# Kernel tuning notes

Measured on AMD Instinct MI355X. Metric: run time of the kernel, lower is better.

Reference implementation:

```python
import jax, jax.numpy as jnp
import numpy as np

B, S, D = 4, 4096, 1024

def setup_inputs() -> dict:
    key = jax.random.key(0)
    ks = jax.random.split(key, 11)
    scale = 1.0 / np.sqrt(D)
    def lin(k):
        return jax.random.normal(k, (D, D), dtype=jnp.float32) * scale
    return {
        "x": jax.random.normal(ks[0], (B, S, D), dtype=jnp.float32),
        "Wq": lin(ks[1]), "bq": jax.random.normal(ks[2], (D,), dtype=jnp.float32) * 0.02,
        "Wk": lin(ks[3]), "bk": jax.random.normal(ks[4], (D,), dtype=jnp.float32) * 0.02,
        "Wv": lin(ks[5]), "bv": jax.random.normal(ks[6], (D,), dtype=jnp.float32) * 0.02,
        "W1": lin(ks[7]), "b1": jax.random.normal(ks[8], (D,), dtype=jnp.float32) * 0.02,
        "W2": lin(ks[9]), "b2": jax.random.normal(ks[10], (D,), dtype=jnp.float32) * 0.02,
    }

def reference(x, Wq, bq, Wk, bk, Wv, bv, W1, b1, W2, b2):
    d = x.shape[-1]
    # Single-head self-attention with residual (faithful to source)
    q = x @ Wq + bq  # [B,S,D]
    k = x @ Wk + bk
    v = x @ Wv + bv
    scores = jnp.einsum('bsd,btd->bst', q, k) / jnp.sqrt(jnp.float32(d))  # [B,S,S]
    attn = jax.nn.softmax(scores, axis=-1)
    x = x + jnp.einsum('bst,btd->bsd', attn, v)
    # FeedForward: fc2(relu(fc1(x))), then doubled (x = x + x in source)
    h = jax.nn.relu(x @ W1 + b1)
    y = h @ W2 + b2
    return y + y
```

## Files before the change

### kernel.cpp

```cpp
#include <hip/hip_runtime.h>
#include <stdint.h>

typedef unsigned short u16;
typedef __bf16 bf16x8 __attribute__((ext_vector_type(8)));
typedef float f32x4 __attribute__((ext_vector_type(4)));
typedef unsigned short u16x8 __attribute__((ext_vector_type(8)));
typedef unsigned short u16x4 __attribute__((ext_vector_type(4)));

__device__ __forceinline__ float b2f(u16 b) {
    return __uint_as_float(((unsigned)b) << 16);
}
__device__ __forceinline__ u16 f2b(float f) {
    unsigned u = __float_as_uint(f);
    unsigned r = (u + 0x7fffu + ((u >> 16) & 1u)) >> 16;
    return (u16)r;
}

#define GLDS16(g, l) __builtin_amdgcn_global_load_lds(                        \
    (const __attribute__((address_space(1))) void*)(g),                       \
    (__attribute__((address_space(3))) void*)(l), 16, 0, 0)

#define BAR()  __builtin_amdgcn_s_barrier()
#define LG0()  do { asm volatile("s_waitcnt lgkmcnt(0)" ::: "memory");        \
                    __builtin_amdgcn_sched_barrier(0); } while (0)
#define VMC(n) asm volatile("s_waitcnt vmcnt(" #n ")" ::: "memory")

template<int HAS_BIAS, int RELU, int HAS_RES, int OUT_MODE>
__device__ __forceinline__ void gemm8_body(
    const u16* __restrict__ A, const u16* __restrict__ Bt,
    const float* __restrict__ bias, const float* __restrict__ res,
    void* __restrict__ Cout, int N, int K,
    long sA, long sB, long sC, long sR, float scale)
{
    __shared__ u16 smem[65536];

    const long nwg = (long)gridDim.x * gridDim.y * gridDim.z;
    long gid = ((long)blockIdx.z * gridDim.y + blockIdx.y) * gridDim.x + blockIdx.x;
    long logical = (nwg % 8 == 0) ? (gid & 7) * (nwg >> 3) + (gid >> 3) : gid;
    const int bx = (int)(logical % gridDim.x);
    long tmp = logical / gridDim.x;
    const int by = (int)(tmp % gridDim.y);
    const int bz = (int)(tmp / gridDim.y);

    A  += (long)bz * sA;
    Bt += (long)bz * sB;

    const int tid  = threadIdx.x;
    const int lane = tid & 63, wid = tid >> 6;
    const int wm   = wid >> 2, wn = wid & 3;
    const int lr   = lane & 15, lk = lane >> 4;
    const long m0  = (long)by * 256;
    const long n0  = (long)bx * 256;
    const int  NT  = K >> 6;

    const u16* gA0 = A  + (m0 + (tid >> 2)) * (long)K + (tid & 3) * 8;
    const u16* gB0 = Bt + (n0 + (tid >> 2)) * (long)K + (tid & 3) * 8;
    const u16* gA1 = gA0 + 128L * K;
    const u16* gB1 = gB0 + 128L * K;
    const int wdst = (tid & ~63) * 8;

#define STA(bufn, kk, kof) do {                                               \
    GLDS16(gA0 + (kof) + (kk) * 32, &smem[(bufn)*16384 + (kk)*8192 + wdst]);  \
    GLDS16(gA1 + (kof) + (kk) * 32, &smem[(bufn)*16384 + (kk)*8192 + wdst + 4096]); } while (0)
#define STB(bufn, kk, kof) do {                                               \
    GLDS16(gB0 + (kof) + (kk) * 32, &smem[32768 + (bufn)*16384 + (kk)*8192 + wdst]); \
    GLDS16(gB1 + (kof) + (kk) * 32, &smem[32768 + (bufn)*16384 + (kk)*8192 + wdst + 4096]); } while (0)

    const int raOff = (wm * 128 + lr) * 32 + lk * 8;
    const int rbOff = (wn * 64  + lr) * 32 + lk * 8;

#define LDA(kk, ih) do { _Pragma("unroll")                                    \
    for (int i = 0; i < 4; ++i)                                               \
        a[i] = *(const bf16x8*)&smem[cur*16384 + (kk)*8192 + raOff + ((ih)*4 + i)*512]; } while (0)
#define LDB(kk) do { _Pragma("unroll")                                        \
    for (int j = 0; j < 4; ++j)                                               \
        b[j] = *(const bf16x8*)&smem[32768 + cur*16384 + (kk)*8192 + rbOff + j*512]; } while (0)
#define MF(ih) do { __builtin_amdgcn_s_setprio(1); _Pragma("unroll")          \
    for (int i = 0; i < 4; ++i) _Pragma("unroll")                             \
        for (int j = 0; j < 4; ++j)                                           \
            acc[(ih)*4 + i][j] = __builtin_amdgcn_mfma_f32_16x16x32_bf16(     \
                a[i], b[j], acc[(ih)*4 + i][j], 0, 0, 0);                     \
    __builtin_amdgcn_s_setprio(0); } while (0)

    f32x4 acc[8][4];
    #pragma unroll
    for (int i = 0; i < 8; ++i)
        #pragma unroll
        for (int j = 0; j < 4; ++j)
            #pragma unroll
            for (int r = 0; r < 4; ++r) acc[i][j][r] = 0.0f;

    bf16x8 a[4], b[4];

    STA(0, 0, 0); STB(0, 0, 0); STA(0, 1, 0); STB(0, 1, 0);
    VMC(4);
    BAR();

    int cur = 0;
    #pragma unroll 1
    for (int t = 0; t < NT - 1; ++t) {
        const long kof = (long)(t + 1) * 64;
        const int nxt = cur ^ 1;
        LDA(0, 0); LDB(0); STA(nxt, 0, kof);
        BAR(); LG0(); MF(0); BAR();
        LDA(0, 1);         STB(nxt, 0, kof);
        BAR(); LG0(); MF(1); VMC(4); BAR();
        LDA(1, 0); LDB(1); STA(nxt, 1, kof);
        BAR(); LG0(); MF(0); BAR();
        LDA(1, 1);         STB(nxt, 1, kof);
        BAR(); LG0(); MF(1); VMC(4); BAR();
        cur = nxt;
    }
    LDA(0, 0); LDB(0); BAR(); LG0(); MF(0); BAR();
    LDA(0, 1);         BAR(); LG0(); MF(1); VMC(0); BAR();
    LDA(1, 0); LDB(1); BAR(); LG0(); MF(0); BAR();
    LDA(1, 1);         BAR(); LG0(); MF(1);

    const long crow0 = m0 + wm * 128;
    const long ccol0 = n0 + wn * 64;
    u16*   Cb = (u16*)Cout   + (long)bz * sC;
    float* Cf = (float*)Cout + (long)bz * sC;
    const float* resz = res + (long)bz * sR;
    #pragma unroll
    for (int i = 0; i < 8; ++i) {
        #pragma unroll
        for (int j = 0; j < 4; ++j) {
            const long col = ccol0 + j * 16 + lr;
            float bv_ = 0.0f;
            if (HAS_BIAS) bv_ = bias[col];
            if (OUT_MODE == 2) {
                const long row0 = crow0 + i * 16 + lk * 4;
                u16x4 pk;
                #pragma unroll
                for (int r = 0; r < 4; ++r) {
                    float v = acc[i][j][r] + bv_;
                    v *= scale;
                    pk[r] = f2b(v);
                }
                const long b_ = row0 >> 12, s_ = row0 & 4095;
                *(u16x4*)((u16*)Cout + (b_ << 22) + (col << 12) + s_) = pk;
            } else {
                #pragma unroll
                for (int r = 0; r < 4; ++r) {
                    const long row = crow0 + i * 16 + lk * 4 + r;
                    float v = acc[i][j][r];
                    if (HAS_BIAS) v += bv_;
                    v *= scale;
                    if (RELU) v = fmaxf(v, 0.0f);
                    if (HAS_RES) v += resz[row * (long)N + col];
                    if (OUT_MODE == 1) Cf[row * (long)N + col] = v;
                    else               Cb[row * (long)N + col] = f2b(v);
                }
            }
        }
    }
#undef STA
#undef STB
#undef LDA
#undef LDB
#undef MF
}

__global__ __launch_bounds__(512, 2) void g8_proj(
    const u16* A, const u16* Bt, const float* bias, u16* C, int N, int K)
{ gemm8_body<1,0,0,0>(A, Bt, bias, nullptr, C, N, K, 0,0,0,0, 1.0f); }

__global__ __launch_bounds__(512, 2) void g8_vproj(
    const u16* A, const u16* Bt, const float* bias, u16* C, int N, int K)
{ gemm8_body<1,0,0,2>(A, Bt, bias, nullptr, C, N, K, 0,0,0,0, 1.0f); }

__global__ __launch_bounds__(512, 2) void g8_qkt(
    const u16* A, const u16* Bt, u16* C, int N, int K,
    long sA, long sB, long sC, float scale)
{ gemm8_body<0,0,0,0>(A, Bt, nullptr, nullptr, C, N, K, sA, sB, sC, 0, scale); }

__global__ __launch_bounds__(512, 2) void g8_pv(
    const u16* A, const u16* Bt, const float* res, u16* C, int N, int K,
    long sA, long sB, long sC, long sR)
{ gemm8_body<0,0,1,0>(A, Bt, nullptr, res, C, N, K, sA, sB, sC, sR, 1.0f); }

__global__ __launch_bounds__(512, 2) void g8_ffn1(
    const u16* A, const u16* Bt, const float* bias, u16* C, int N, int K)
{ gemm8_body<1,1,0,0>(A, Bt, bias, nullptr, C, N, K, 0,0,0,0, 1.0f); }

__global__ __launch_bounds__(512, 2) void g8_ffn2(
    const u16* A, const u16* Bt, const float* bias, float* C, int N, int K, float scale)
{ gemm8_body<1,0,0,1>(A, Bt, bias, nullptr, C, N, K, 0,0,0,0, scale); }

__global__ __launch_bounds__(256) void cvt_f32_bf16(
    const float* __restrict__ in, u16* __restrict__ out, long n)
{
    long i = ((long)blockIdx.x * 256 + threadIdx.x) * 4;
    if (i >= n) return;
    float4 f = *(const float4*)(in + i);
    u16x4 o;
    o[0] = f2b(f.x); o[1] = f2b(f.y); o[2] = f2b(f.z); o[3] = f2b(f.w);
    *(u16x4*)(out + i) = o;
}

__global__ __launch_bounds__(256) void transpose_to_bf16(
    const float* __restrict__ in, u16* __restrict__ out, int R, int C)
{
    __shared__ float tile[32][33];
    const int bx = blockIdx.x * 32;
    const int by = blockIdx.y * 32;
    const int tx = threadIdx.x, ty = threadIdx.y;
    #pragma unroll
    for (int i = 0; i < 32; i += 8)
        tile[ty + i][tx] = in[(long)(by + ty + i) * C + bx + tx];
    __syncthreads();
    #pragma unroll
    for (int i = 0; i < 32; i += 8)
        out[(long)(bx + ty + i) * R + by + tx] = f2b(tile[tx][ty + i]);
}

__global__ __launch_bounds__(256) void softmax_rows(u16* __restrict__ P, int n)
{
    const int t = threadIdx.x;
    const int lane = t & 63, w = t >> 6;
    u16* row = P + (long)blockIdx.x * n;
    u16x8 a = *(const u16x8*)(row + t * 16);
    u16x8 b = *(const u16x8*)(row + t * 16 + 8);
    float v[16];
    #pragma unroll
    for (int i = 0; i < 8; ++i) { v[i] = b2f(a[i]); v[8 + i] = b2f(b[i]); }

    float mx = v[0];
    #pragma unroll
    for (int i = 1; i < 16; ++i) mx = fmaxf(mx, v[i]);
    #pragma unroll
    for (int o = 32; o > 0; o >>= 1) mx = fmaxf(mx, __shfl_xor(mx, o));
    __shared__ float red[8];
    if (lane == 0) red[w] = mx;
    __syncthreads();
    mx = fmaxf(fmaxf(red[0], red[1]), fmaxf(red[2], red[3]));

    float s = 0.0f;
    #pragma unroll
    for (int i = 0; i < 16; ++i) { v[i] = __expf(v[i] - mx); s += v[i]; }
    #pragma unroll
    for (int o = 32; o > 0; o >>= 1) s += __shfl_xor(s, o);
    if (lane == 0) red[4 + w] = s;
    __syncthreads();
    s = red[4] + red[5] + red[6] + red[7];
    const float inv = 1.0f / s;

    #pragma unroll
    for (int i = 0; i < 8; ++i) { a[i] = f2b(v[i] * inv); b[i] = f2b(v[8 + i] * inv); }
    *(u16x8*)(row + t * 16)     = a;
    *(u16x8*)(row + t * 16 + 8) = b;
}

extern "C" void kernel_launch(void* const* d_in, const int* in_sizes, int n_in,
                              void* d_out, int out_size, void* d_ws, size_t ws_size,
                              hipStream_t stream)
{
    (void)in_sizes; (void)n_in; (void)out_size;
    const float* x  = (const float*)d_in[0];
    const float* Wq = (const float*)d_in[1];
    const float* bq = (const float*)d_in[2];
    const float* Wk = (const float*)d_in[3];
    const float* bk = (const float*)d_in[4];
    const float* Wv = (const float*)d_in[5];
    const float* bv = (const float*)d_in[6];
    const float* W1 = (const float*)d_in[7];
    const float* b1 = (const float*)d_in[8];
    const float* W2 = (const float*)d_in[9];
    const float* b2 = (const float*)d_in[10];
    float* out = (float*)d_out;

    const int  B = 4, S = 4096, D = 1024;
    const long SD  = (long)S * D;
    const long BSD = (long)B * SD;
    const long SS  = (long)S * S;

    int BC = 4;
    while (BC > 1 && (size_t)((long)BC * SS + 5L * D * D + 3L * BSD) * 2 > ws_size)
        BC >>= 1;

    u16* Pb = (u16*)d_ws;
    u16* xb = Pb;
    u16* Wt = Pb + (long)BC * SS;
    u16* Qb = Wt + 5L * D * D;
    u16* Kb = Qb + BSD;
    u16* Vt = Kb + BSD;

    cvt_f32_bf16<<<dim3((unsigned)(BSD / 4 / 256)), 256, 0, stream>>>(x, xb, BSD);

    dim3 tb(32, 8);
    transpose_to_bf16<<<dim3(D / 32, D / 32), tb, 0, stream>>>(Wq, Wt + 0L * D * D, D, D);
    transpose_to_bf16<<<dim3(D / 32, D / 32), tb, 0, stream>>>(Wk, Wt + 1L * D * D, D, D);
    transpose_to_bf16<<<dim3(D / 32, D / 32), tb, 0, stream>>>(Wv, Wt + 2L * D * D, D, D);
    transpose_to_bf16<<<dim3(D / 32, D / 32), tb, 0, stream>>>(W1, Wt + 3L * D * D, D, D);
    transpose_to_bf16<<<dim3(D / 32, D / 32), tb, 0, stream>>>(W2, Wt + 4L * D * D, D, D);

    const dim3 gproj(D / 256, (B * S) / 256);
    g8_proj <<<gproj, 512, 0, stream>>>(xb, Wt + 0L*D*D, bq, Qb, D, D);
    g8_proj <<<gproj, 512, 0, stream>>>(xb, Wt + 1L*D*D, bk, Kb, D, D);
    g8_vproj<<<gproj, 512, 0, stream>>>(xb, Wt + 2L*D*D, bv, Vt, D, D);

    for (int c = 0; c < B; c += BC) {
        g8_qkt<<<dim3(S/256, S/256, BC), 512, 0, stream>>>(
            Qb + (long)c * SD, Kb + (long)c * SD, Pb, S, D, SD, SD, SS, 0.03125f);
        softmax_rows<<<BC * S, 256, 0, stream>>>(Pb, S);
        g8_pv<<<dim3(D/256, S/256, BC), 512, 0, stream>>>(
            Pb, Vt + (long)c * SD, x + (long)c * SD, Kb + (long)c * SD,
            D, S, SS, SD, SD, SD);
    }

    g8_ffn1<<<gproj, 512, 0, stream>>>(Kb, Wt + 3L*D*D, b1, Qb, D, D);
    g8_ffn2<<<gproj, 512, 0, stream>>>(Qb, Wt + 4L*D*D, b2, out, D, D, 2.0f);
}
```

Measured before the change: 536.0 us.

## Double-buffer LDS fragment registers to overlap ds_reads with MFMA in GEMM mainloop

Rewrites the GEMM mainloop into a software-pipelined schedule. Two register sets of A/B fragments are kept, so LDS reads for the next sub-step are issued before the MFMAs of the current one. Partial lgkmcnt waits replace full drains, and the four barriers per half-tile become two vmcnt+barrier checkpoints per K tile. This removes LDS-read latency stalls and barrier overhead, at the cost of extra VGPRs for the second fragment set and tighter ordering assumptions between buffer reuse and global-to-LDS loads.

```diff
diff --git a/kernel.cpp b/kernel.cpp
--- a/kernel.cpp
+++ b/kernel.cpp
@@ -20,13 +20,8 @@
     (const __attribute__((address_space(1))) void*)(g),                       \
     (__attribute__((address_space(3))) void*)(l), 16, 0, 0)
 
-#define BAR()  __builtin_amdgcn_s_barrier()
-#define LG0()  do { asm volatile("s_waitcnt lgkmcnt(0)" ::: "memory");        \
-                    __builtin_amdgcn_sched_barrier(0); } while (0)
-#define VMC(n) asm volatile("s_waitcnt vmcnt(" #n ")" ::: "memory")
-
 template<int HAS_BIAS, int RELU, int HAS_RES, int OUT_MODE>
-__device__ __forceinline__ void gemm8_body(
+__device__ __forceinline__ void gemm9_body(
     const u16* __restrict__ A, const u16* __restrict__ Bt,
     const float* __restrict__ bias, const float* __restrict__ res,
     void* __restrict__ Cout, int N, int K,
@@ -69,18 +64,48 @@
     const int raOff = (wm * 128 + lr) * 32 + lk * 8;
     const int rbOff = (wn * 64  + lr) * 32 + lk * 8;
 
-#define LDA(kk, ih) do { _Pragma("unroll")                                    \
+#define DSA(dst, BUF, kk, ih) do { _Pragma("unroll")                          \
     for (int i = 0; i < 4; ++i)                                               \
-        a[i] = *(const bf16x8*)&smem[cur*16384 + (kk)*8192 + raOff + ((ih)*4 + i)*512]; } while (0)
-#define LDB(kk) do { _Pragma("unroll")                                        \
+        dst[i] = *(const bf16x8*)&smem[(BUF)*16384 + (kk)*8192 + raOff + ((ih)*4 + i)*512]; } while (0)
+#define DSB(dst, BUF, kk) do { _Pragma("unroll")                              \
     for (int j = 0; j < 4; ++j)                                               \
-        b[j] = *(const bf16x8*)&smem[32768 + cur*16384 + (kk)*8192 + rbOff + j*512]; } while (0)
-#define MF(ih) do { __builtin_amdgcn_s_setprio(1); _Pragma("unroll")          \
+        dst[j] = *(const bf16x8*)&smem[32768 + (BUF)*16384 + (kk)*8192 + rbOff + j*512]; } while (0)
+
+#define LGK(n) do { asm volatile("s_waitcnt lgkmcnt(" #n ")" ::: "memory");   \
+                    __builtin_amdgcn_sched_barrier(0); } while (0)
+#define CKPT(n) do { asm volatile("s_waitcnt vmcnt(" #n ")" ::: "memory");    \
+    __builtin_amdgcn_s_barrier(); __builtin_amdgcn_sched_barrier(0); } while (0)
+
+#define MFM(IH, A_, B_) do { __builtin_amdgcn_s_setprio(1); _Pragma("unroll") \
     for (int i = 0; i < 4; ++i) _Pragma("unroll")                             \
         for (int j = 0; j < 4; ++j)                                           \
-            acc[(ih)*4 + i][j] = __builtin_amdgcn_mfma_f32_16x16x32_bf16(     \
-                a[i], b[j], acc[(ih)*4 + i][j], 0, 0, 0);                     \
+            acc[(IH)*4 + i][j] = __builtin_amdgcn_mfma_f32_16x16x32_bf16(     \
+                A_[i], B_[j], acc[(IH)*4 + i][j], 0, 0, 0);                   \
     __builtin_amdgcn_s_setprio(0); } while (0)
+
+#define TILE_MAIN(BUF, kof) do {                                              \
+    DSA(aY, BUF, 0, 1);                 STA((BUF)^1, 0, kof);                 \
+    LGK(4);  MFM(0, aX, bX);                                                  \
+    CKPT(2);                                                                  \
+    DSA(aX, BUF, 1, 0);  DSB(bY, BUF, 1);  STB((BUF)^1, 0, kof);              \
+    LGK(8);  MFM(1, aY, bX);                                                  \
+    DSA(aY, BUF, 1, 1);                 STA((BUF)^1, 1, kof);                 \
+    LGK(4);  MFM(0, aX, bY);                                                  \
+    CKPT(2);                                                                  \
+    DSA(aX, (BUF)^1, 0, 0);  DSB(bX, (BUF)^1, 0);  STB((BUF)^1, 1, kof);      \
+    LGK(8);  MFM(1, aY, bY);                                                  \
+} while (0)
+
+#define TILE_LAST(BUF) do {                                                   \
+    DSA(aY, BUF, 0, 1);                                                       \
+    LGK(4);  MFM(0, aX, bX);                                                  \
+    CKPT(0);                                                                  \
+    DSA(aX, BUF, 1, 0);  DSB(bY, BUF, 1);                                     \
+    LGK(8);  MFM(1, aY, bX);                                                  \
+    DSA(aY, BUF, 1, 1);                                                       \
+    LGK(4);  MFM(0, aX, bY);                                                  \
+    LGK(0);  MFM(1, aY, bY);                                                  \
+} while (0)
 
     f32x4 acc[8][4];
     #pragma unroll
@@ -90,31 +115,19 @@
             #pragma unroll
             for (int r = 0; r < 4; ++r) acc[i][j][r] = 0.0f;
 
-    bf16x8 a[4], b[4];
+    bf16x8 aX[4], aY[4], bX[4], bY[4];
 
     STA(0, 0, 0); STB(0, 0, 0); STA(0, 1, 0); STB(0, 1, 0);
-    VMC(4);
-    BAR();
-
-    int cur = 0;
+    CKPT(4);
+    DSA(aX, 0, 0, 0); DSB(bX, 0, 0);
+
     #pragma unroll 1
-    for (int t = 0; t < NT - 1; ++t) {
-        const long kof = (long)(t + 1) * 64;
-        const int nxt = cur ^ 1;
-        LDA(0, 0); LDB(0); STA(nxt, 0, kof);
-        BAR(); LG0(); MF(0); BAR();
-        LDA(0, 1);         STB(nxt, 0, kof);
-        BAR(); LG0(); MF(1); VMC(4); BAR();
-        LDA(1, 0); LDB(1); STA(nxt, 1, kof);
-        BAR(); LG0(); MF(0); BAR();
-        LDA(1, 1);         STB(nxt, 1, kof);
-        BAR(); LG0(); MF(1); VMC(4); BAR();
-        cur = nxt;
+    for (int t = 0; t + 2 < NT; t += 2) {
+        TILE_MAIN(0, (long)(t + 1) * 64);
+        TILE_MAIN(1, (long)(t + 2) * 64);
     }
-    LDA(0, 0); LDB(0); BAR(); LG0(); MF(0); BAR();
-    LDA(0, 1);         BAR(); LG0(); MF(1); VMC(0); BAR();
-    LDA(1, 0); LDB(1); BAR(); LG0(); MF(0); BAR();
-    LDA(1, 1);         BAR(); LG0(); MF(1);
+    TILE_MAIN(0, (long)(NT - 1) * 64);
+    TILE_LAST(1);
 
     const long crow0 = m0 + wm * 128;
     const long ccol0 = n0 + wn * 64;
@@ -156,36 +169,40 @@
     }
 #undef STA
 #undef STB
-#undef LDA
-#undef LDB
-#undef MF
-}
-
-__global__ __launch_bounds__(512, 2) void g8_proj(
+#undef DSA
+#undef DSB
+#undef LGK
+#undef CKPT
+#undef MFM
+#undef TILE_MAIN
+#undef TILE_LAST
+}
+
+__global__ __launch_bounds__(512, 2) void g9_proj(
     const u16* A, const u16* Bt, const float* bias, u16* C, int N, int K)
-{ gemm8_body<1,0,0,0>(A, Bt, bias, nullptr, C, N, K, 0,0,0,0, 1.0f); }
-
-__global__ __launch_bounds__(512, 2) void g8_vproj(
+{ gemm9_body<1,0,0,0>(A, Bt, bias, nullptr, C, N, K, 0,0,0,0, 1.0f); }
+
+__global__ __launch_bounds__(512, 2) void g9_vproj(
     const u16* A, const u16* Bt, const float* bias, u16* C, int N, int K)
-{ gemm8_body<1,0,0,2>(A, Bt, bias, nullptr, C, N, K, 0,0,0,0, 1.0f); }
-
-__global__ __launch_bounds__(512, 2) void g8_qkt(
+{ gemm9_body<1,0,0,2>(A, Bt, bias, nullptr, C, N, K, 0,0,0,0, 1.0f); }
+
+__global__ __launch_bounds__(512, 2) void g9_qkt(
     const u16* A, const u16* Bt, u16* C, int N, int K,
     long sA, long sB, long sC, float scale)
-{ gemm8_body<0,0,0,0>(A, Bt, nullptr, nullptr, C, N, K, sA, sB, sC, 0, scale); }
-
-__global__ __launch_bounds__(512, 2) void g8_pv(
+{ gemm9_body<0,0,0,0>(A, Bt, nullptr, nullptr, C, N, K, sA, sB, sC, 0, scale); }
+
+__global__ __launch_bounds__(512, 2) void g9_pv(
     const u16* A, const u16* Bt, const float* res, u16* C, int N, int K,
     long sA, long sB, long sC, long sR)
-{ gemm8_body<0,0,1,0>(A, Bt, nullptr, res, C, N, K, sA, sB, sC, sR, 1.0f); }
-
-__global__ __launch_bounds__(512, 2) void g8_ffn1(
+{ gemm9_body<0,0,1,0>(A, Bt, nullptr, res, C, N, K, sA, sB, sC, sR, 1.0f); }
+
+__global__ __launch_bounds__(512, 2) void g9_ffn1(
     const u16* A, const u16* Bt, const float* bias, u16* C, int N, int K)
-{ gemm8_body<1,1,0,0>(A, Bt, bias, nullptr, C, N, K, 0,0,0,0, 1.0f); }
-
-__global__ __launch_bounds__(512, 2) void g8_ffn2(
+{ gemm9_body<1,1,0,0>(A, Bt, bias, nullptr, C, N, K, 0,0,0,0, 1.0f); }
+
+__global__ __launch_bounds__(512, 2) void g9_ffn2(
     const u16* A, const u16* Bt, const float* bias, float* C, int N, int K, float scale)
-{ gemm8_body<1,0,0,1>(A, Bt, bias, nullptr, C, N, K, 0,0,0,0, scale); }
+{ gemm9_body<1,0,0,1>(A, Bt, bias, nullptr, C, N, K, 0,0,0,0, scale); }
 
 __global__ __launch_bounds__(256) void cvt_f32_bf16(
     const float* __restrict__ in, u16* __restrict__ out, long n)
@@ -295,19 +312,19 @@
     transpose_to_bf16<<<dim3(D / 32, D / 32), tb, 0, stream>>>(W2, Wt + 4L * D * D, D, D);
 
     const dim3 gproj(D / 256, (B * S) / 256);
-    g8_proj <<<gproj, 512, 0, stream>>>(xb, Wt + 0L*D*D, bq, Qb, D, D);
-    g8_proj <<<gproj, 512, 0, stream>>>(xb, Wt + 1L*D*D, bk, Kb, D, D);
-    g8_vproj<<<gproj, 512, 0, stream>>>(xb, Wt + 2L*D*D, bv, Vt, D, D);
+    g9_proj <<<gproj, 512, 0, stream>>>(xb, Wt + 0L*D*D, bq, Qb, D, D);
+    g9_proj <<<gproj, 512, 0, stream>>>(xb, Wt + 1L*D*D, bk, Kb, D, D);
+    g9_vproj<<<gproj, 512, 0, stream>>>(xb, Wt + 2L*D*D, bv, Vt, D, D);
 
     for (int c = 0; c < B; c += BC) {
-        g8_qkt<<<dim3(S/256, S/256, BC), 512, 0, stream>>>(
+        g9_qkt<<<dim3(S/256, S/256, BC), 512, 0, stream>>>(
             Qb + (long)c * SD, Kb + (long)c * SD, Pb, S, D, SD, SD, SS, 0.03125f);
         softmax_rows<<<BC * S, 256, 0, stream>>>(Pb, S);
-        g8_pv<<<dim3(D/256, S/256, BC), 512, 0, stream>>>(
+        g9_pv<<<dim3(D/256, S/256, BC), 512, 0, stream>>>(
             Pb, Vt + (long)c * SD, x + (long)c * SD, Kb + (long)c * SD,
             D, S, SS, SD, SD, SD);
     }
 
-    g8_ffn1<<<gproj, 512, 0, stream>>>(Kb, Wt + 3L*D*D, b1, Qb, D, D);
-    g8_ffn2<<<gproj, 512, 0, stream>>>(Qb, Wt + 4L*D*D, b2, out, D, D, 2.0f);
-}
+    g9_ffn1<<<gproj, 512, 0, stream>>>(Kb, Wt + 3L*D*D, b1, Qb, D, D);
+    g9_ffn2<<<gproj, 512, 0, stream>>>(Qb, Wt + 4L*D*D, b2, out, D, D, 2.0f);
+}
```

After: 546.2 us. No clear change (+1.9%).

## Swizzle LDS layout and reorder GEMM MFMA quarters for operand reuse

Applied to the files above, without the earlier changes.

Applies an XOR swizzle to the k-chunk placement in shared memory, on both the global-to-LDS load side and the fragment read side, to cut LDS bank conflicts. It also reorganizes the inner loop to load all 8 A fragments once per k-half and split the work across N halves in serpentine order, so each B fragment half is reused and fewer LDS reads are issued. The peeled epilogue iteration is folded into the main loop behind conditionals. Holding 8 A fragments raises register pressure, and the extra branches could disturb scheduling.

```diff
diff --git a/kernel.cpp b/kernel.cpp
--- a/kernel.cpp
+++ b/kernel.cpp
@@ -23,10 +23,11 @@
 #define BAR()  __builtin_amdgcn_s_barrier()
 #define LG0()  do { asm volatile("s_waitcnt lgkmcnt(0)" ::: "memory");        \
                     __builtin_amdgcn_sched_barrier(0); } while (0)
-#define VMC(n) asm volatile("s_waitcnt vmcnt(" #n ")" ::: "memory")
+#define WVM4() asm volatile("s_waitcnt vmcnt(4)" ::: "memory")
+#define WVM0() asm volatile("s_waitcnt vmcnt(0)" ::: "memory")
 
 template<int HAS_BIAS, int RELU, int HAS_RES, int OUT_MODE>
-__device__ __forceinline__ void gemm8_body(
+__device__ __forceinline__ void gemm13_body(
     const u16* __restrict__ A, const u16* __restrict__ Bt,
     const float* __restrict__ bias, const float* __restrict__ res,
     void* __restrict__ Cout, int N, int K,
@@ -53,33 +54,36 @@
     const long n0  = (long)bx * 256;
     const int  NT  = K >> 6;
 
-    const u16* gA0 = A  + (m0 + (tid >> 2)) * (long)K + (tid & 3) * 8;
-    const u16* gB0 = Bt + (n0 + (tid >> 2)) * (long)K + (tid & 3) * 8;
+    const int sch = ((tid & 3) ^ ((tid >> 3) & 3)) * 8;
+    const u16* gA0 = A  + (m0 + (tid >> 2)) * (long)K + sch;
+    const u16* gB0 = Bt + (n0 + (tid >> 2)) * (long)K + sch;
     const u16* gA1 = gA0 + 128L * K;
     const u16* gB1 = gB0 + 128L * K;
     const int wdst = (tid & ~63) * 8;
 
-#define STA(bufn, kk, kof) do {                                               \
-    GLDS16(gA0 + (kof) + (kk) * 32, &smem[(bufn)*16384 + (kk)*8192 + wdst]);  \
-    GLDS16(gA1 + (kof) + (kk) * 32, &smem[(bufn)*16384 + (kk)*8192 + wdst + 4096]); } while (0)
-#define STB(bufn, kk, kof) do {                                               \
-    GLDS16(gB0 + (kof) + (kk) * 32, &smem[32768 + (bufn)*16384 + (kk)*8192 + wdst]); \
-    GLDS16(gB1 + (kof) + (kk) * 32, &smem[32768 + (bufn)*16384 + (kk)*8192 + wdst + 4096]); } while (0)
-
-    const int raOff = (wm * 128 + lr) * 32 + lk * 8;
-    const int rbOff = (wn * 64  + lr) * 32 + lk * 8;
-
-#define LDA(kk, ih) do { _Pragma("unroll")                                    \
-    for (int i = 0; i < 4; ++i)                                               \
-        a[i] = *(const bf16x8*)&smem[cur*16384 + (kk)*8192 + raOff + ((ih)*4 + i)*512]; } while (0)
-#define LDB(kk) do { _Pragma("unroll")                                        \
-    for (int j = 0; j < 4; ++j)                                               \
-        b[j] = *(const bf16x8*)&smem[32768 + cur*16384 + (kk)*8192 + rbOff + j*512]; } while (0)
-#define MF(ih) do { __builtin_amdgcn_s_setprio(1); _Pragma("unroll")          \
-    for (int i = 0; i < 4; ++i) _Pragma("unroll")                             \
-        for (int j = 0; j < 4; ++j)                                           \
-            acc[(ih)*4 + i][j] = __builtin_amdgcn_mfma_f32_16x16x32_bf16(     \
-                a[i], b[j], acc[(ih)*4 + i][j], 0, 0, 0);                     \
+#define STA(bufn, kh, kof) do {                                               \
+    GLDS16(gA0 + (kof) + (kh) * 32, &smem[(bufn)*16384 + (kh)*8192 + wdst]);  \
+    GLDS16(gA1 + (kof) + (kh) * 32, &smem[(bufn)*16384 + (kh)*8192 + wdst + 4096]); } while (0)
+#define STB(bufn, kh, kof) do {                                               \
+    GLDS16(gB0 + (kof) + (kh) * 32, &smem[32768 + (bufn)*16384 + (kh)*8192 + wdst]); \
+    GLDS16(gB1 + (kof) + (kh) * 32, &smem[32768 + (bufn)*16384 + (kh)*8192 + wdst + 4096]); } while (0)
+
+    const int lkA    = lk ^ ((lr >> 1) & 3);
+    const int raBase = (wm * 128 + lr) * 32 + lkA * 8;
+    const int rbBase = (wn * 64  + lr) * 32 + lkA * 8;
+
+#define LDA(c, kh) do { _Pragma("unroll")                                     \
+    for (int i = 0; i < 8; ++i)                                               \
+        a[i] = *(const bf16x8*)&smem[(c)*16384 + (kh)*8192 + raBase + i*512]; } while (0)
+#define LDB(c, kh, nh) do { _Pragma("unroll")                                 \
+    for (int jj = 0; jj < 2; ++jj)                                            \
+        b[jj] = *(const bf16x8*)&smem[32768 + (c)*16384 + (kh)*8192 + rbBase + (nh)*1024 + jj*512]; } while (0)
+
+#define MFMA_Q(nh) do { __builtin_amdgcn_s_setprio(1); _Pragma("unroll")      \
+    for (int i = 0; i < 8; ++i) _Pragma("unroll")                             \
+        for (int jj = 0; jj < 2; ++jj)                                        \
+            acc[i][(nh)*2 + jj] = __builtin_amdgcn_mfma_f32_16x16x32_bf16(    \
+                a[i], b[jj], acc[i][(nh)*2 + jj], 0, 0, 0);                   \
     __builtin_amdgcn_s_setprio(0); } while (0)
 
     f32x4 acc[8][4];
@@ -90,31 +94,40 @@
             #pragma unroll
             for (int r = 0; r < 4; ++r) acc[i][j][r] = 0.0f;
 
-    bf16x8 a[4], b[4];
-
     STA(0, 0, 0); STB(0, 0, 0); STA(0, 1, 0); STB(0, 1, 0);
-    VMC(4);
+    WVM4();
     BAR();
 
-    int cur = 0;
     #pragma unroll 1
-    for (int t = 0; t < NT - 1; ++t) {
-        const long kof = (long)(t + 1) * 64;
-        const int nxt = cur ^ 1;
-        LDA(0, 0); LDB(0); STA(nxt, 0, kof);
-        BAR(); LG0(); MF(0); BAR();
-        LDA(0, 1);         STB(nxt, 0, kof);
-        BAR(); LG0(); MF(1); VMC(4); BAR();
-        LDA(1, 0); LDB(1); STA(nxt, 1, kof);
-        BAR(); LG0(); MF(0); BAR();
-        LDA(1, 1);         STB(nxt, 1, kof);
-        BAR(); LG0(); MF(1); VMC(4); BAR();
-        cur = nxt;
+    for (int t = 0; t < NT; ++t) {
+        const int cur = t & 1, nxt = cur ^ 1;
+        const long kN = (long)(t + 1) * 64;
+        const bool st = (t + 1 < NT);
+        bf16x8 a[8], b[2];
+
+        LDA(cur, 0); LDB(cur, 0, 0);
+        if (st) STA(nxt, 0, kN);
+        BAR(); LG0();
+        MFMA_Q(0);
+        BAR();
+        LDB(cur, 0, 1);
+        if (st) STB(nxt, 0, kN);
+        BAR(); LG0();
+        MFMA_Q(1);
+        if (st) { WVM4(); } else { WVM0(); }
+        BAR();
+        LDA(cur, 1); LDB(cur, 1, 1);
+        if (st) STA(nxt, 1, kN);
+        BAR(); LG0();
+        MFMA_Q(1);
+        BAR();
+        LDB(cur, 1, 0);
+        if (st) STB(nxt, 1, kN);
+        BAR(); LG0();
+        MFMA_Q(0);
+        if (st) { WVM4(); } else { WVM0(); }
+        BAR();
     }
-    LDA(0, 0); LDB(0); BAR(); LG0(); MF(0); BAR();
-    LDA(0, 1);         BAR(); LG0(); MF(1); VMC(0); BAR();
-    LDA(1, 0); LDB(1); BAR(); LG0(); MF(0); BAR();
-    LDA(1, 1);         BAR(); LG0(); MF(1);
 
     const long crow0 = m0 + wm * 128;
     const long ccol0 = n0 + wn * 64;
@@ -158,34 +171,34 @@
 #undef STB
 #undef LDA
 #undef LDB
-#undef MF
-}
-
-__global__ __launch_bounds__(512, 2) void g8_proj(
+#undef MFMA_Q
+}
+
+__global__ __launch_bounds__(512, 2) void g13_proj(
     const u16* A, const u16* Bt, const float* bias, u16* C, int N, int K)
-{ gemm8_body<1,0,0,0>(A, Bt, bias, nullptr, C, N, K, 0,0,0,0, 1.0f); }
-
-__global__ __launch_bounds__(512, 2) void g8_vproj(
+{ gemm13_body<1,0,0,0>(A, Bt, bias, nullptr, C, N, K, 0,0,0,0, 1.0f); }
+
+__global__ __launch_bounds__(512, 2) void g13_vproj(
     const u16* A, const u16* Bt, const float* bias, u16* C, int N, int K)
-{ gemm8_body<1,0,0,2>(A, Bt, bias, nullptr, C, N, K, 0,0,0,0, 1.0f); }
-
-__global__ __launch_bounds__(512, 2) void g8_qkt(
+{ gemm13_body<1,0,0,2>(A, Bt, bias, nullptr, C, N, K, 0,0,0,0, 1.0f); }
+
+__global__ __launch_bounds__(512, 2) void g13_qkt(
     const u16* A, const u16* Bt, u16* C, int N, int K,
     long sA, long sB, long sC, float scale)
-{ gemm8_body<0,0,0,0>(A, Bt, nullptr, nullptr, C, N, K, sA, sB, sC, 0, scale); }
-
-__global__ __launch_bounds__(512, 2) void g8_pv(
+{ gemm13_body<0,0,0,0>(A, Bt, nullptr, nullptr, C, N, K, sA, sB, sC, 0, scale); }
+
+__global__ __launch_bounds__(512, 2) void g13_pv(
     const u16* A, const u16* Bt, const float* res, u16* C, int N, int K,
     long sA, long sB, long sC, long sR)
-{ gemm8_body<0,0,1,0>(A, Bt, nullptr, res, C, N, K, sA, sB, sC, sR, 1.0f); }
-
-__global__ __launch_bounds__(512, 2) void g8_ffn1(
+{ gemm13_body<0,0,1,0>(A, Bt, nullptr, res, C, N, K, sA, sB, sC, sR, 1.0f); }
+
+__global__ __launch_bounds__(512, 2) void g13_ffn1(
     const u16* A, const u16* Bt, const float* bias, u16* C, int N, int K)
-{ gemm8_body<1,1,0,0>(A, Bt, bias, nullptr, C, N, K, 0,0,0,0, 1.0f); }
-
-__global__ __launch_bounds__(512, 2) void g8_ffn2(
+{ gemm13_body<1,1,0,0>(A, Bt, bias, nullptr, C, N, K, 0,0,0,0, 1.0f); }
+
+__global__ __launch_bounds__(512, 2) void g13_ffn2(
     const u16* A, const u16* Bt, const float* bias, float* C, int N, int K, float scale)
-{ gemm8_body<1,0,0,1>(A, Bt, bias, nullptr, C, N, K, 0,0,0,0, scale); }
+{ gemm13_body<1,0,0,1>(A, Bt, bias, nullptr, C, N, K, 0,0,0,0, scale); }
 
 __global__ __launch_bounds__(256) void cvt_f32_bf16(
     const float* __restrict__ in, u16* __restrict__ out, long n)
@@ -295,19 +308,19 @@
     transpose_to_bf16<<<dim3(D / 32, D / 32), tb, 0, stream>>>(W2, Wt + 4L * D * D, D, D);
 
     const dim3 gproj(D / 256, (B * S) / 256);
-    g8_proj <<<gproj, 512, 0, stream>>>(xb, Wt + 0L*D*D, bq, Qb, D, D);
-    g8_proj <<<gproj, 512, 0, stream>>>(xb, Wt + 1L*D*D, bk, Kb, D, D);
-    g8_vproj<<<gproj, 512, 0, stream>>>(xb, Wt + 2L*D*D, bv, Vt, D, D);
+    g13_proj <<<gproj, 512, 0, stream>>>(xb, Wt + 0L*D*D, bq, Qb, D, D);
+    g13_proj <<<gproj, 512, 0, stream>>>(xb, Wt + 1L*D*D, bk, Kb, D, D);
+    g13_vproj<<<gproj, 512, 0, stream>>>(xb, Wt + 2L*D*D, bv, Vt, D, D);
 
     for (int c = 0; c < B; c += BC) {
-        g8_qkt<<<dim3(S/256, S/256, BC), 512, 0, stream>>>(
+        g13_qkt<<<dim3(S/256, S/256, BC), 512, 0, stream>>>(
             Qb + (long)c * SD, Kb + (long)c * SD, Pb, S, D, SD, SD, SS, 0.03125f);
         softmax_rows<<<BC * S, 256, 0, stream>>>(Pb, S);
-        g8_pv<<<dim3(D/256, S/256, BC), 512, 0, stream>>>(
+        g13_pv<<<dim3(D/256, S/256, BC), 512, 0, stream>>>(
             Pb, Vt + (long)c * SD, x + (long)c * SD, Kb + (long)c * SD,
             D, S, SS, SD, SD, SD);
     }
 
-    g8_ffn1<<<gproj, 512, 0, stream>>>(Kb, Wt + 3L*D*D, b1, Qb, D, D);
-    g8_ffn2<<<gproj, 512, 0, stream>>>(Qb, Wt + 4L*D*D, b2, out, D, D, 2.0f);
-}
+    g13_ffn1<<<gproj, 512, 0, stream>>>(Kb, Wt + 3L*D*D, b1, Qb, D, D);
+    g13_ffn2<<<gproj, 512, 0, stream>>>(Qb, Wt + 4L*D*D, b2, out, D, D, 2.0f);
+}
```

New measurement: 530.5 us. Within noise of the previous version (-1.0%).
